# Performance work log

Hardware: AMD Instinct MI355X
Metric: run time of the kernel (lower is better)

## Reference

```python
import jax, jax.numpy as jnp
import numpy as np

D = 1024      # input_dim
NH = 16       # num_heads
HD = D // NH  # head_dim = 64
B, S = 2, 2048


def setup_inputs() -> dict:
    key = jax.random.key(0)
    ks = jax.random.split(key, 12)
    scale = 1.0 / np.sqrt(D)
    inp = {
        "query": jax.random.normal(ks[0], (B, S, D), jnp.float32),
        "key": jax.random.normal(ks[1], (B, S, D), jnp.float32),
        "value": jax.random.normal(ks[2], (B, S, D), jnp.float32),
        # Linear weights stored as [in, out] so y = x @ W + b
        "Wq": jax.random.normal(ks[3], (D, D), jnp.float32) * scale,
        "bq": jnp.zeros((D,), jnp.float32),
        "Wk": jax.random.normal(ks[4], (D, D), jnp.float32) * scale,
        "bk": jnp.zeros((D,), jnp.float32),
        "Wv": jax.random.normal(ks[5], (D, D), jnp.float32) * scale,
        "bv": jnp.zeros((D,), jnp.float32),
        "Wo": jax.random.normal(ks[6], (D, D), jnp.float32) * scale,
        "bo": jnp.zeros((D,), jnp.float32),
    }
    return inp


def reference(query, key, value, Wq, bq, Wk, bk, Wv, bv, Wo, bo):
    b, s, _ = query.shape
    q = query @ Wq + bq
    k = key @ Wk + bk
    v = value @ Wv + bv
    # NOTE: module reshapes to (b, s, head_dim, num_heads) -- heads LAST
    q = q.reshape(b, s, HD, NH)
    k = k.reshape(b, s, HD, NH)
    v = v.reshape(b, s, HD, NH)
    # contract over head_dim d; result [b, l, n, h]
    scores = jnp.einsum('bldh,bndh->blnh', q, k) / jnp.sqrt(jnp.float32(HD))
    # Softmax(dim=-1) in the original acts over the HEAD axis (faithful)
    probs = jax.nn.softmax(scores, axis=-1)
    out = jnp.einsum('blnh,bndh->bldh', probs, v).reshape(b, s, D)
    out = out @ Wo + bo
    return (out, probs)
```

## Files before the change

### kernel.cpp

```cpp
#include <hip/hip_runtime.h>

#define DD   1024
#define NHH  16
#define HDD  64
#define BB   2
#define SS   2048
#define MT   (BB*SS)
#define BL   16
#define BN   32

typedef __attribute__((ext_vector_type(8))) __bf16 bf16x8;
typedef __attribute__((ext_vector_type(4))) float  floatx4;
typedef __attribute__((ext_vector_type(4))) short  shortx4;

static __device__ __forceinline__ short bf16_of(float f) {
    unsigned u = __builtin_bit_cast(unsigned, f);
    u = (u + 0x7fffu + ((u >> 16) & 1u)) >> 16;
    return (short)u;
}

__global__ void cast_f32_to_bf16(const float* __restrict__ in,
                                 short* __restrict__ out, int n4) {
    int i = blockIdx.x * blockDim.x + threadIdx.x;
    if (i >= n4) return;
    floatx4 f = ((const floatx4*)in)[i];
    shortx4 o;
    o[0] = bf16_of(f[0]); o[1] = bf16_of(f[1]);
    o[2] = bf16_of(f[2]); o[3] = bf16_of(f[3]);
    ((shortx4*)out)[i] = o;
}

__global__ void transpose_cast_w(const float* __restrict__ W,
                                 short* __restrict__ Wt) {
    __shared__ float tile[32][33];
    int tx = threadIdx.x & 31, ty = threadIdx.x >> 5;
    int o0 = blockIdx.x * 32, i0 = blockIdx.y * 32;
#pragma unroll
    for (int r = 0; r < 32; r += 8)
        tile[ty + r][tx] = W[(size_t)(i0 + ty + r) * DD + o0 + tx];
    __syncthreads();
#pragma unroll
    for (int r = 0; r < 32; r += 8)
        Wt[(size_t)(o0 + ty + r) * DD + i0 + tx] = bf16_of(tile[tx][ty + r]);
}

__global__ __launch_bounds__(256) void gemm_proj(
    const short* __restrict__ X, const short* __restrict__ Wt,
    const float* __restrict__ bias, short* __restrict__ out, int vmode) {
    int wave = threadIdx.x >> 6, lane = threadIdx.x & 63;
    int quad = lane >> 4, lr = lane & 15;
    int m0 = blockIdx.x * 64 + (wave >> 1) * 32;
    int n0 = blockIdx.y * 64 + (wave & 1) * 32;
    floatx4 acc[2][2] = {};
    for (int k0 = 0; k0 < DD; k0 += 32) {
        bf16x8 a[2], bfr[2];
#pragma unroll
        for (int mb = 0; mb < 2; mb++)
            a[mb] = *(const bf16x8*)(X + (size_t)(m0 + mb*16 + lr) * DD + k0 + quad*8);
#pragma unroll
        for (int nb = 0; nb < 2; nb++)
            bfr[nb] = *(const bf16x8*)(Wt + (size_t)(n0 + nb*16 + lr) * DD + k0 + quad*8);
#pragma unroll
        for (int mb = 0; mb < 2; mb++)
#pragma unroll
            for (int nb = 0; nb < 2; nb++)
                acc[mb][nb] = __builtin_amdgcn_mfma_f32_16x16x32_bf16(
                    a[mb], bfr[nb], acc[mb][nb], 0, 0, 0);
    }
#pragma unroll
    for (int mb = 0; mb < 2; mb++)
#pragma unroll
    for (int nb = 0; nb < 2; nb++)
#pragma unroll
    for (int r = 0; r < 4; r++) {
        int m = m0 + mb*16 + quad*4 + r;
        int n = n0 + nb*16 + lr;
        float y = acc[mb][nb][r] + bias[n];
        int b = m >> 11, l = m & (SS - 1);
        int h = n & (NHH - 1), d = n >> 4;
        size_t idx;
        if (vmode == 0) idx = (((size_t)(b*NHH + h) * SS) + l) * HDD + d;
        else            idx = (((size_t)(b*NHH + h) * HDD) + d) * SS + l;
        out[idx] = bf16_of(y);
    }
}

__global__ __launch_bounds__(256) void gemm_outp(
    const short* __restrict__ X, const short* __restrict__ Wt,
    const float* __restrict__ bias, float* __restrict__ out) {
    int wave = threadIdx.x >> 6, lane = threadIdx.x & 63;
    int quad = lane >> 4, lr = lane & 15;
    int m0 = blockIdx.x * 64 + (wave >> 1) * 32;
    int n0 = blockIdx.y * 64 + (wave & 1) * 32;
    floatx4 acc[2][2] = {};
    for (int k0 = 0; k0 < DD; k0 += 32) {
        bf16x8 a[2], bfr[2];
#pragma unroll
        for (int mb = 0; mb < 2; mb++)
            a[mb] = *(const bf16x8*)(X + (size_t)(m0 + mb*16 + lr) * DD + k0 + quad*8);
#pragma unroll
        for (int nb = 0; nb < 2; nb++)
            bfr[nb] = *(const bf16x8*)(Wt + (size_t)(n0 + nb*16 + lr) * DD + k0 + quad*8);
#pragma unroll
        for (int mb = 0; mb < 2; mb++)
#pragma unroll
            for (int nb = 0; nb < 2; nb++)
                acc[mb][nb] = __builtin_amdgcn_mfma_f32_16x16x32_bf16(
                    a[mb], bfr[nb], acc[mb][nb], 0, 0, 0);
    }
#pragma unroll
    for (int mb = 0; mb < 2; mb++)
#pragma unroll
    for (int nb = 0; nb < 2; nb++)
#pragma unroll
    for (int r = 0; r < 4; r++) {
        int m = m0 + mb*16 + quad*4 + r;
        int n = n0 + nb*16 + lr;
        out[(size_t)m * DD + n] = acc[mb][nb][r] + bias[n];
    }
}

__global__ __launch_bounds__(1024) void attn_fused(
    const short* __restrict__ qws, const short* __restrict__ kws,
    const short* __restrict__ vtws, float* __restrict__ probs,
    short* __restrict__ aout) {
    __shared__ float sm[NHH * 528];
    int h = threadIdx.x >> 6, lane = threadIdx.x & 63;
    int quad = lane >> 4, lr = lane & 15;
    int b  = blockIdx.x >> 7;
    int l0 = (blockIdx.x & 127) * BL;

    const short* qh = qws  + ((size_t)(b*NHH + h) * SS) * HDD;
    const short* kh = kws  + ((size_t)(b*NHH + h) * SS) * HDD;
    const short* vh = vtws + ((size_t)(b*NHH + h) * HDD) * SS;

    bf16x8 aq0 = *(const bf16x8*)(qh + (size_t)(l0 + lr) * HDD + quad*8);
    bf16x8 aq1 = *(const bf16x8*)(qh + (size_t)(l0 + lr) * HDD + 32 + quad*8);

    floatx4 acco[4] = {};

    for (int nt = 0; nt < SS / BN; nt++) {
        int n0 = nt * BN;
#pragma unroll
        for (int nb = 0; nb < 2; nb++) {
            bf16x8 bk0 = *(const bf16x8*)(kh + (size_t)(n0 + nb*16 + lr) * HDD + quad*8);
            bf16x8 bk1 = *(const bf16x8*)(kh + (size_t)(n0 + nb*16 + lr) * HDD + 32 + quad*8);
            floatx4 s = {};
            s = __builtin_amdgcn_mfma_f32_16x16x32_bf16(aq0, bk0, s, 0, 0, 0);
            s = __builtin_amdgcn_mfma_f32_16x16x32_bf16(aq1, bk1, s, 0, 0, 0);
#pragma unroll
            for (int r = 0; r < 4; r++) {
                int ll = quad*4 + r, nn = nb*16 + lr;
                sm[h*528 + ll*33 + nn] = s[r] * 0.125f;
            }
        }
        __syncthreads();
        if (threadIdx.x < BL*BN) {
            int ll = threadIdx.x >> 5, nn = threadIdx.x & 31;
            int base = ll*33 + nn;
            float p[16];
            float mx = -1e30f;
#pragma unroll
            for (int i = 0; i < 16; i++) { p[i] = sm[i*528 + base]; mx = fmaxf(mx, p[i]); }
            float sum = 0.f;
#pragma unroll
            for (int i = 0; i < 16; i++) { p[i] = __expf(p[i] - mx); sum += p[i]; }
            float inv = 1.f / sum;
            float* gp = probs + ((size_t)(b*SS + l0 + ll) * SS + n0 + nn) * NHH;
#pragma unroll
            for (int i = 0; i < 16; i++) { p[i] *= inv; sm[i*528 + base] = p[i]; }
#pragma unroll
            for (int i = 0; i < 4; i++) {
                floatx4 t; t[0]=p[4*i]; t[1]=p[4*i+1]; t[2]=p[4*i+2]; t[3]=p[4*i+3];
                ((floatx4*)gp)[i] = t;
            }
        }
        __syncthreads();
        union { short s[8]; bf16x8 v; } apu;
#pragma unroll
        for (int j = 0; j < 8; j++)
            apu.s[j] = bf16_of(sm[h*528 + lr*33 + quad*8 + j]);
#pragma unroll
        for (int db = 0; db < 4; db++) {
            bf16x8 bv = *(const bf16x8*)(vh + (size_t)(db*16 + lr) * SS + n0 + quad*8);
            acco[db] = __builtin_amdgcn_mfma_f32_16x16x32_bf16(apu.v, bv, acco[db], 0, 0, 0);
        }
        __syncthreads();
    }
#pragma unroll
    for (int db = 0; db < 4; db++)
#pragma unroll
    for (int r = 0; r < 4; r++) {
        int ll = quad*4 + r, d = db*16 + lr;
        aout[(size_t)(b*SS + l0 + ll) * DD + d*NHH + h] = bf16_of(acco[db][r]);
    }
}

extern "C" void kernel_launch(void* const* d_in, const int* in_sizes, int n_in,
                              void* d_out, int out_size, void* d_ws, size_t ws_size,
                              hipStream_t stream) {
    const float* query = (const float*)d_in[0];
    const float* key_  = (const float*)d_in[1];
    const float* value = (const float*)d_in[2];
    const float* Wq = (const float*)d_in[3];
    const float* bq = (const float*)d_in[4];
    const float* Wk = (const float*)d_in[5];
    const float* bk = (const float*)d_in[6];
    const float* Wv = (const float*)d_in[7];
    const float* bv = (const float*)d_in[8];
    const float* Wo = (const float*)d_in[9];
    const float* bo = (const float*)d_in[10];

    float* out   = (float*)d_out;
    float* probs = out + (size_t)MT * DD;

    const size_t SZ_X = (size_t)MT * DD;
    const size_t SZ_W = (size_t)DD * DD;
    short* ws   = (short*)d_ws;
    short* xq   = ws;
    short* xk   = xq + SZ_X;
    short* xv   = xk + SZ_X;
    short* wtq  = xv + SZ_X;
    short* wtk  = wtq + SZ_W;
    short* wtv  = wtk + SZ_W;
    short* wto  = wtv + SZ_W;
    short* qws  = wto + SZ_W;
    short* kws  = qws + SZ_X;
    short* vtws = kws + SZ_X;
    short* aout = vtws + SZ_X;

    int n4 = (int)(SZ_X / 4);
    cast_f32_to_bf16<<<n4 / 256, 256, 0, stream>>>(query, xq, n4);
    cast_f32_to_bf16<<<n4 / 256, 256, 0, stream>>>(key_,  xk, n4);
    cast_f32_to_bf16<<<n4 / 256, 256, 0, stream>>>(value, xv, n4);

    transpose_cast_w<<<dim3(32, 32), 256, 0, stream>>>(Wq, wtq);
    transpose_cast_w<<<dim3(32, 32), 256, 0, stream>>>(Wk, wtk);
    transpose_cast_w<<<dim3(32, 32), 256, 0, stream>>>(Wv, wtv);
    transpose_cast_w<<<dim3(32, 32), 256, 0, stream>>>(Wo, wto);

    gemm_proj<<<dim3(64, 16), 256, 0, stream>>>(xq, wtq, bq, qws, 0);
    gemm_proj<<<dim3(64, 16), 256, 0, stream>>>(xk, wtk, bk, kws, 0);
    gemm_proj<<<dim3(64, 16), 256, 0, stream>>>(xv, wtv, bv, vtws, 1);

    attn_fused<<<BB * (SS / BL), 1024, 0, stream>>>(qws, kws, vtws, probs, aout);

    gemm_outp<<<dim3(64, 16), 256, 0, stream>>>(aout, wto, bo, out);
}
```

Measured before the change: 1.193 ms.

## Tile GEMMs through LDS with async loads and split attention over keys

Replaces the projection and output GEMMs with one LDS-tiled kernel that stages 128x32 A and 64x32 B tiles through global_load_lds, so each block reuses them across more output. The attention kernel's key range is split into two chunks, doubling the grid from 256 blocks. Each chunk writes fp32 partial outputs through a shared-memory transpose, and a new reduce kernel sums them into bf16. The split costs an extra fp32 round trip through global memory and one more launch. The workspace is reordered so the partials reuse the dead input-cast buffers.

```diff
diff --git a/kernel.cpp b/kernel.cpp
--- a/kernel.cpp
+++ b/kernel.cpp
@@ -8,6 +8,7 @@
 #define MT   (BB*SS)
 #define BL   16
 #define BN   32
+#define NSPLIT 2
 
 typedef __attribute__((ext_vector_type(8))) __bf16 bf16x8;
 typedef __attribute__((ext_vector_type(4))) float  floatx4;
@@ -17,6 +18,13 @@
     unsigned u = __builtin_bit_cast(unsigned, f);
     u = (u + 0x7fffu + ((u >> 16) & 1u)) >> 16;
     return (short)u;
+}
+
+static __device__ __forceinline__ void async_copy16(const short* g, short* l) {
+    __builtin_amdgcn_global_load_lds(
+        (const __attribute__((address_space(1))) unsigned int*)g,
+        (__attribute__((address_space(3))) unsigned int*)l,
+        16, 0, 0);
 }
 
 __global__ void cast_f32_to_bf16(const float* __restrict__ in,
@@ -44,156 +52,166 @@
         Wt[(size_t)(o0 + ty + r) * DD + i0 + tx] = bf16_of(tile[tx][ty + r]);
 }
 
-__global__ __launch_bounds__(256) void gemm_proj(
+__global__ __launch_bounds__(256) void gemm_tiled(
     const short* __restrict__ X, const short* __restrict__ Wt,
-    const float* __restrict__ bias, short* __restrict__ out, int vmode) {
-    int wave = threadIdx.x >> 6, lane = threadIdx.x & 63;
+    const float* __restrict__ bias, void* __restrict__ out, int mode) {
+    __shared__ short As[128 * 32];
+    __shared__ short Bs[64 * 32];
+    int t = threadIdx.x;
+    int wave = t >> 6, lane = t & 63;
     int quad = lane >> 4, lr = lane & 15;
-    int m0 = blockIdx.x * 64 + (wave >> 1) * 32;
-    int n0 = blockIdx.y * 64 + (wave & 1) * 32;
-    floatx4 acc[2][2] = {};
+    int wm = wave & 1, wn = wave >> 1;
+    int m0 = blockIdx.x * 128, n0 = blockIdx.y * 64;
+
+    int arow = t >> 2, acol = (t & 3) * 8;
+    floatx4 acc[4][2] = {};
+
     for (int k0 = 0; k0 < DD; k0 += 32) {
-        bf16x8 a[2], bfr[2];
-#pragma unroll
-        for (int mb = 0; mb < 2; mb++)
-            a[mb] = *(const bf16x8*)(X + (size_t)(m0 + mb*16 + lr) * DD + k0 + quad*8);
-#pragma unroll
-        for (int nb = 0; nb < 2; nb++)
-            bfr[nb] = *(const bf16x8*)(Wt + (size_t)(n0 + nb*16 + lr) * DD + k0 + quad*8);
-#pragma unroll
-        for (int mb = 0; mb < 2; mb++)
-#pragma unroll
-            for (int nb = 0; nb < 2; nb++)
-                acc[mb][nb] = __builtin_amdgcn_mfma_f32_16x16x32_bf16(
-                    a[mb], bfr[nb], acc[mb][nb], 0, 0, 0);
-    }
-#pragma unroll
-    for (int mb = 0; mb < 2; mb++)
-#pragma unroll
-    for (int nb = 0; nb < 2; nb++)
+        async_copy16(X + (size_t)(m0 + arow) * DD + k0 + acol,       As + t * 8);
+        async_copy16(X + (size_t)(m0 + 64 + arow) * DD + k0 + acol,  As + 2048 + t * 8);
+        async_copy16(Wt + (size_t)(n0 + arow) * DD + k0 + acol,      Bs + t * 8);
+        __syncthreads();
+        bf16x8 a[4], bb[2];
+#pragma unroll
+        for (int mi = 0; mi < 4; mi++)
+            a[mi] = *(const bf16x8*)(As + (wm * 64 + mi * 16 + lr) * 32 + quad * 8);
+#pragma unroll
+        for (int ni = 0; ni < 2; ni++)
+            bb[ni] = *(const bf16x8*)(Bs + (wn * 32 + ni * 16 + lr) * 32 + quad * 8);
+#pragma unroll
+        for (int mi = 0; mi < 4; mi++)
+#pragma unroll
+            for (int ni = 0; ni < 2; ni++)
+                acc[mi][ni] = __builtin_amdgcn_mfma_f32_16x16x32_bf16(
+                    a[mi], bb[ni], acc[mi][ni], 0, 0, 0);
+        __syncthreads();
+    }
+
+#pragma unroll
+    for (int mi = 0; mi < 4; mi++)
+#pragma unroll
+    for (int ni = 0; ni < 2; ni++)
 #pragma unroll
     for (int r = 0; r < 4; r++) {
-        int m = m0 + mb*16 + quad*4 + r;
-        int n = n0 + nb*16 + lr;
-        float y = acc[mb][nb][r] + bias[n];
-        int b = m >> 11, l = m & (SS - 1);
-        int h = n & (NHH - 1), d = n >> 4;
-        size_t idx;
-        if (vmode == 0) idx = (((size_t)(b*NHH + h) * SS) + l) * HDD + d;
-        else            idx = (((size_t)(b*NHH + h) * HDD) + d) * SS + l;
-        out[idx] = bf16_of(y);
-    }
-}
-
-__global__ __launch_bounds__(256) void gemm_outp(
-    const short* __restrict__ X, const short* __restrict__ Wt,
-    const float* __restrict__ bias, float* __restrict__ out) {
-    int wave = threadIdx.x >> 6, lane = threadIdx.x & 63;
-    int quad = lane >> 4, lr = lane & 15;
-    int m0 = blockIdx.x * 64 + (wave >> 1) * 32;
-    int n0 = blockIdx.y * 64 + (wave & 1) * 32;
-    floatx4 acc[2][2] = {};
-    for (int k0 = 0; k0 < DD; k0 += 32) {
-        bf16x8 a[2], bfr[2];
-#pragma unroll
-        for (int mb = 0; mb < 2; mb++)
-            a[mb] = *(const bf16x8*)(X + (size_t)(m0 + mb*16 + lr) * DD + k0 + quad*8);
-#pragma unroll
-        for (int nb = 0; nb < 2; nb++)
-            bfr[nb] = *(const bf16x8*)(Wt + (size_t)(n0 + nb*16 + lr) * DD + k0 + quad*8);
-#pragma unroll
-        for (int mb = 0; mb < 2; mb++)
-#pragma unroll
-            for (int nb = 0; nb < 2; nb++)
-                acc[mb][nb] = __builtin_amdgcn_mfma_f32_16x16x32_bf16(
-                    a[mb], bfr[nb], acc[mb][nb], 0, 0, 0);
-    }
-#pragma unroll
-    for (int mb = 0; mb < 2; mb++)
-#pragma unroll
-    for (int nb = 0; nb < 2; nb++)
-#pragma unroll
-    for (int r = 0; r < 4; r++) {
-        int m = m0 + mb*16 + quad*4 + r;
-        int n = n0 + nb*16 + lr;
-        out[(size_t)m * DD + n] = acc[mb][nb][r] + bias[n];
+        int m = m0 + wm * 64 + mi * 16 + quad * 4 + r;
+        int n = n0 + wn * 32 + ni * 16 + lr;
+        float y = acc[mi][ni][r] + bias[n];
+        if (mode == 2) {
+            ((float*)out)[(size_t)m * DD + n] = y;
+        } else {
+            int b = m >> 11, l = m & (SS - 1);
+            int h = n & (NHH - 1), d = n >> 4;
+            size_t idx;
+            if (mode == 0) idx = (((size_t)(b * NHH + h) * SS) + l) * HDD + d;
+            else           idx = (((size_t)(b * NHH + h) * HDD) + d) * SS + l;
+            ((short*)out)[idx] = bf16_of(y);
+        }
     }
 }
 
 __global__ __launch_bounds__(1024) void attn_fused(
     const short* __restrict__ qws, const short* __restrict__ kws,
     const short* __restrict__ vtws, float* __restrict__ probs,
-    short* __restrict__ aout) {
+    float* __restrict__ partial) {
     __shared__ float sm[NHH * 528];
     int h = threadIdx.x >> 6, lane = threadIdx.x & 63;
     int quad = lane >> 4, lr = lane & 15;
-    int b  = blockIdx.x >> 7;
-    int l0 = (blockIdx.x & 127) * BL;
-
-    const short* qh = qws  + ((size_t)(b*NHH + h) * SS) * HDD;
-    const short* kh = kws  + ((size_t)(b*NHH + h) * SS) * HDD;
-    const short* vh = vtws + ((size_t)(b*NHH + h) * HDD) * SS;
-
-    bf16x8 aq0 = *(const bf16x8*)(qh + (size_t)(l0 + lr) * HDD + quad*8);
-    bf16x8 aq1 = *(const bf16x8*)(qh + (size_t)(l0 + lr) * HDD + 32 + quad*8);
+    int c    = blockIdx.x & (NSPLIT - 1);
+    int l0   = ((blockIdx.x >> 1) & 127) * BL;
+    int b    = blockIdx.x >> 8;
+
+    const short* qh = qws  + ((size_t)(b * NHH + h) * SS) * HDD;
+    const short* kh = kws  + ((size_t)(b * NHH + h) * SS) * HDD;
+    const short* vh = vtws + ((size_t)(b * NHH + h) * HDD) * SS;
+
+    bf16x8 aq0 = *(const bf16x8*)(qh + (size_t)(l0 + lr) * HDD + quad * 8);
+    bf16x8 aq1 = *(const bf16x8*)(qh + (size_t)(l0 + lr) * HDD + 32 + quad * 8);
 
     floatx4 acco[4] = {};
-
-    for (int nt = 0; nt < SS / BN; nt++) {
+    const int NT = (SS / BN) / NSPLIT;
+
+    for (int nt = c * NT; nt < (c + 1) * NT; nt++) {
         int n0 = nt * BN;
 #pragma unroll
         for (int nb = 0; nb < 2; nb++) {
-            bf16x8 bk0 = *(const bf16x8*)(kh + (size_t)(n0 + nb*16 + lr) * HDD + quad*8);
-            bf16x8 bk1 = *(const bf16x8*)(kh + (size_t)(n0 + nb*16 + lr) * HDD + 32 + quad*8);
+            bf16x8 bk0 = *(const bf16x8*)(kh + (size_t)(n0 + nb * 16 + lr) * HDD + quad * 8);
+            bf16x8 bk1 = *(const bf16x8*)(kh + (size_t)(n0 + nb * 16 + lr) * HDD + 32 + quad * 8);
             floatx4 s = {};
             s = __builtin_amdgcn_mfma_f32_16x16x32_bf16(aq0, bk0, s, 0, 0, 0);
             s = __builtin_amdgcn_mfma_f32_16x16x32_bf16(aq1, bk1, s, 0, 0, 0);
 #pragma unroll
             for (int r = 0; r < 4; r++) {
-                int ll = quad*4 + r, nn = nb*16 + lr;
-                sm[h*528 + ll*33 + nn] = s[r] * 0.125f;
+                int ll = quad * 4 + r, nn = nb * 16 + lr;
+                sm[h * 528 + ll * 33 + nn] = s[r] * 0.125f;
             }
         }
         __syncthreads();
-        if (threadIdx.x < BL*BN) {
+        if (threadIdx.x < BL * BN) {
             int ll = threadIdx.x >> 5, nn = threadIdx.x & 31;
-            int base = ll*33 + nn;
+            int base = ll * 33 + nn;
             float p[16];
             float mx = -1e30f;
 #pragma unroll
-            for (int i = 0; i < 16; i++) { p[i] = sm[i*528 + base]; mx = fmaxf(mx, p[i]); }
+            for (int i = 0; i < 16; i++) { p[i] = sm[i * 528 + base]; mx = fmaxf(mx, p[i]); }
             float sum = 0.f;
 #pragma unroll
             for (int i = 0; i < 16; i++) { p[i] = __expf(p[i] - mx); sum += p[i]; }
             float inv = 1.f / sum;
-            float* gp = probs + ((size_t)(b*SS + l0 + ll) * SS + n0 + nn) * NHH;
-#pragma unroll
-            for (int i = 0; i < 16; i++) { p[i] *= inv; sm[i*528 + base] = p[i]; }
+            float* gp = probs + ((size_t)(b * SS + l0 + ll) * SS + n0 + nn) * NHH;
+#pragma unroll
+            for (int i = 0; i < 16; i++) { p[i] *= inv; sm[i * 528 + base] = p[i]; }
 #pragma unroll
             for (int i = 0; i < 4; i++) {
-                floatx4 t; t[0]=p[4*i]; t[1]=p[4*i+1]; t[2]=p[4*i+2]; t[3]=p[4*i+3];
-                ((floatx4*)gp)[i] = t;
+                floatx4 tv; tv[0]=p[4*i]; tv[1]=p[4*i+1]; tv[2]=p[4*i+2]; tv[3]=p[4*i+3];
+                ((floatx4*)gp)[i] = tv;
             }
         }
         __syncthreads();
         union { short s[8]; bf16x8 v; } apu;
 #pragma unroll
         for (int j = 0; j < 8; j++)
-            apu.s[j] = bf16_of(sm[h*528 + lr*33 + quad*8 + j]);
+            apu.s[j] = bf16_of(sm[h * 528 + lr * 33 + quad * 8 + j]);
 #pragma unroll
         for (int db = 0; db < 4; db++) {
-            bf16x8 bv = *(const bf16x8*)(vh + (size_t)(db*16 + lr) * SS + n0 + quad*8);
+            bf16x8 bv = *(const bf16x8*)(vh + (size_t)(db * 16 + lr) * SS + n0 + quad * 8);
             acco[db] = __builtin_amdgcn_mfma_f32_16x16x32_bf16(apu.v, bv, acco[db], 0, 0, 0);
         }
         __syncthreads();
     }
-#pragma unroll
-    for (int db = 0; db < 4; db++)
-#pragma unroll
-    for (int r = 0; r < 4; r++) {
-        int ll = quad*4 + r, d = db*16 + lr;
-        aout[(size_t)(b*SS + l0 + ll) * DD + d*NHH + h] = bf16_of(acco[db][r]);
-    }
+
+    float* pc = partial + (size_t)c * MT * DD;
+#pragma unroll
+    for (int half = 0; half < 2; half++) {
+#pragma unroll
+        for (int db2 = 0; db2 < 2; db2++) {
+            int db = half * 2 + db2;
+#pragma unroll
+            for (int r = 0; r < 4; r++) {
+                int ll = quad * 4 + r;
+                int dloc = db2 * 16 + lr;
+                sm[ll * 528 + dloc * 16 + h] = acco[db][r];
+            }
+        }
+        __syncthreads();
+        int l  = threadIdx.x >> 6;
+        int c0 = (threadIdx.x & 63) * 8;
+        float* dst = pc + (size_t)(b * SS + l0 + l) * DD + half * 512 + c0;
+        const float* srcp = &sm[l * 528 + c0];
+        ((floatx4*)dst)[0] = ((const floatx4*)srcp)[0];
+        ((floatx4*)dst)[1] = ((const floatx4*)srcp)[1];
+        __syncthreads();
+    }
+}
+
+__global__ void reduce_partials(const float* __restrict__ pa,
+                                short* __restrict__ aout) {
+    size_t i = (size_t)blockIdx.x * blockDim.x + threadIdx.x;
+    floatx4 a = ((const floatx4*)pa)[i];
+    floatx4 b = ((const floatx4*)pa)[i + (size_t)MT * DD / 4];
+    shortx4 o;
+    o[0] = bf16_of(a[0] + b[0]); o[1] = bf16_of(a[1] + b[1]);
+    o[2] = bf16_of(a[2] + b[2]); o[3] = bf16_of(a[3] + b[3]);
+    ((shortx4*)aout)[i] = o;
 }
 
 extern "C" void kernel_launch(void* const* d_in, const int* in_sizes, int n_in,
@@ -217,17 +235,18 @@
     const size_t SZ_X = (size_t)MT * DD;
     const size_t SZ_W = (size_t)DD * DD;
     short* ws   = (short*)d_ws;
-    short* xq   = ws;
+    short* wto  = ws;
+    short* qws  = wto + SZ_W;
+    short* kws  = qws + SZ_X;
+    short* vtws = kws + SZ_X;
+    short* aout = vtws + SZ_X;
+    short* xq   = aout + SZ_X;
     short* xk   = xq + SZ_X;
     short* xv   = xk + SZ_X;
     short* wtq  = xv + SZ_X;
     short* wtk  = wtq + SZ_W;
     short* wtv  = wtk + SZ_W;
-    short* wto  = wtv + SZ_W;
-    short* qws  = wto + SZ_W;
-    short* kws  = qws + SZ_X;
-    short* vtws = kws + SZ_X;
-    short* aout = vtws + SZ_X;
+    float* partial = (float*)xq;
 
     int n4 = (int)(SZ_X / 4);
     cast_f32_to_bf16<<<n4 / 256, 256, 0, stream>>>(query, xq, n4);
@@ -239,11 +258,13 @@
     transpose_cast_w<<<dim3(32, 32), 256, 0, stream>>>(Wv, wtv);
     transpose_cast_w<<<dim3(32, 32), 256, 0, stream>>>(Wo, wto);
 
-    gemm_proj<<<dim3(64, 16), 256, 0, stream>>>(xq, wtq, bq, qws, 0);
-    gemm_proj<<<dim3(64, 16), 256, 0, stream>>>(xk, wtk, bk, kws, 0);
-    gemm_proj<<<dim3(64, 16), 256, 0, stream>>>(xv, wtv, bv, vtws, 1);
-
-    attn_fused<<<BB * (SS / BL), 1024, 0, stream>>>(qws, kws, vtws, probs, aout);
-
-    gemm_outp<<<dim3(64, 16), 256, 0, stream>>>(aout, wto, bo, out);
-}
+    gemm_tiled<<<dim3(32, 16), 256, 0, stream>>>(xq, wtq, bq, qws, 0);
+    gemm_tiled<<<dim3(32, 16), 256, 0, stream>>>(xk, wtk, bk, kws, 0);
+    gemm_tiled<<<dim3(32, 16), 256, 0, stream>>>(xv, wtv, bv, vtws, 1);
+
+    attn_fused<<<BB * (SS / BL) * NSPLIT, 1024, 0, stream>>>(qws, kws, vtws, probs, partial);
+
+    reduce_partials<<<(int)(SZ_X / 4 / 256), 256, 0, stream>>>(partial, aout);
+
+    gemm_tiled<<<dim3(32, 16), 256, 0, stream>>>(aout, wto, bo, out, 2);
+}
```

Result: faster. 1.062 ms (-11.0%).
